# Kernel tuning notes

Measured on AMD Instinct MI355X. Metric: run time of the kernel, lower is better.

Reference implementation:

```python
import jax, jax.numpy as jnp
import numpy as np

HIDDEN = 2048
HEADS = 16
HEAD_DIM = HIDDEN // HEADS  # 128
ROPE_BASE = 10000.0
RMS_EPS = 1e-6
MINUS_INF = -10000.0


def rms_norm(x, w):
    xf = x.astype(jnp.float32)
    var = jnp.mean(xf * xf, axis=-1, keepdims=True)
    return w * (x * jax.lax.rsqrt(var + RMS_EPS))


def rotate_half(x):
    x1, x2 = jnp.split(x, 2, axis=-1)
    return jnp.concatenate((-x2, x1), axis=-1)


def rope_tables(seq_len, dtype):
    inv_freq = 1.0 / (ROPE_BASE ** (jnp.arange(0, HEAD_DIM, 2, dtype=jnp.float32) / HEAD_DIM))
    t = jnp.arange(seq_len, dtype=jnp.float32)
    freqs = jnp.einsum('i,j->ij', t, inv_freq)           # [S, D/2]
    emb = jnp.concatenate((freqs, freqs), axis=-1)       # [S, D]
    return jnp.cos(emb).astype(dtype), jnp.sin(emb).astype(dtype)


def setup_inputs() -> dict:
    key = jax.random.key(0)
    ks = jax.random.split(key, 6)
    B, S, H = 2, 2048, HIDDEN
    x = jax.random.normal(ks[0], (B, S, H), dtype=jnp.float32) * 0.5
    norm_w = jnp.ones((H,), dtype=jnp.float32)
    scale = 0.02
    wq = jax.random.normal(ks[1], (H, H), dtype=jnp.float32) * scale
    wk = jax.random.normal(ks[2], (H, H), dtype=jnp.float32) * scale
    wv = jax.random.normal(ks[3], (H, H), dtype=jnp.float32) * scale
    wo = jax.random.normal(ks[4], (H, H), dtype=jnp.float32) * scale
    position_ids = jnp.broadcast_to(jnp.arange(S, dtype=jnp.int32), (B, S))
    return {"x": x, "norm_w": norm_w, "wq": wq, "wk": wk, "wv": wv,
            "wo": wo, "position_ids": position_ids}


def reference(x, norm_w, wq, wk, wv, wo, position_ids):
    B, S, H = x.shape
    h = rms_norm(x, norm_w)
    # torch Linear: y = h @ W.T, weight is [out, in]
    def proj(w):
        return jnp.einsum('bsd,od->bso', h, w).reshape(B, S, HEADS, HEAD_DIM).transpose(0, 2, 1, 3)
    q, k, v = proj(wq), proj(wk), proj(wv)  # [B, Hh, S, D]
    cos, sin = rope_tables(S, x.dtype)
    cos = cos[position_ids][:, None]  # [B, 1, S, D]
    sin = sin[position_ids][:, None]
    q = q * cos + rotate_half(q) * sin
    k = k * cos + rotate_half(k) * sin
    scores = jnp.einsum('bhqd,bhkd->bhqk', q, k) / jnp.sqrt(jnp.float32(HEAD_DIM))
    causal = jnp.tril(jnp.ones((S, S), dtype=bool))
    scores = scores + jnp.where(causal, 0.0, MINUS_INF).astype(scores.dtype)
    probs = jax.nn.softmax(scores, axis=-1)
    ctx = jnp.einsum('bhqk,bhkd->bhqd', probs, v)          # [B, Hh, S, D]
    ctx = ctx.transpose(0, 2, 1, 3).reshape(B, S, H)
    out = jnp.einsum('bsd,od->bso', ctx, wo)
    return out
```

## Files before the change

kernel.cpp:

```cpp
#include <hip/hip_runtime.h>
#include <hip/hip_bf16.h>
#include <stdint.h>

#define S_LEN   2048
#define BATCH   2
#define HID     2048
#define NHEADS  16
#define HDIM    128
#define ROWS    (BATCH * S_LEN)
#define QKS     4096
#define ATT_SCALE 0.08838834764831843f
#define LOG2E     1.4426950408889634f

typedef __attribute__((ext_vector_type(8))) short s16x8;
typedef __attribute__((ext_vector_type(4))) float f32x4;

#define GLL16(gp, lp)                                                          \
  __builtin_amdgcn_global_load_lds(                                            \
      (__attribute__((address_space(1))) void*)(gp),                           \
      (__attribute__((address_space(3))) void*)(lp), 16, 0, 0)

__device__ __forceinline__ float bf2f(unsigned short u) {
  union { unsigned int i; float f; } v; v.i = ((unsigned int)u) << 16; return v.f;
}
__device__ __forceinline__ unsigned short f2bf(float f) {
  union { float f; unsigned int i; } v; v.f = f;
  unsigned int i = v.i;
  return (unsigned short)((i + 0x7FFFu + ((i >> 16) & 1u)) >> 16);
}
__device__ __forceinline__ void store_out(unsigned short* p, float v) { *p = f2bf(v); }
__device__ __forceinline__ void store_out(float* p, float v) { *p = v; }

__global__ __launch_bounds__(256) void cast4_kernel(const float* __restrict__ w0,
                                                    const float* __restrict__ w1,
                                                    const float* __restrict__ w2,
                                                    const float* __restrict__ w3,
                                                    unsigned short* __restrict__ dqkv,
                                                    unsigned short* __restrict__ dwo) {
  const int which = blockIdx.y;
  const float* src = (which == 0) ? w0 : (which == 1) ? w1 : (which == 2) ? w2 : w3;
  unsigned short* dst = (which < 3) ? dqkv + (size_t)which * HID * HID : dwo;
  int i = blockIdx.x * 256 + threadIdx.x;
  float4 v = ((const float4*)src)[i];
  ushort4 o;
  o.x = f2bf(v.x); o.y = f2bf(v.y); o.z = f2bf(v.z); o.w = f2bf(v.w);
  ((ushort4*)dst)[i] = o;
}

__global__ __launch_bounds__(256) void rmsnorm_kernel(const float* __restrict__ x,
                                                      const float* __restrict__ w,
                                                      unsigned short* __restrict__ h) {
  int row = blockIdx.x;
  int t = threadIdx.x;
  const float4* xr4 = (const float4*)(x + (size_t)row * HID);
  float4 a = xr4[t], b = xr4[t + 256];
  float ss = a.x*a.x + a.y*a.y + a.z*a.z + a.w*a.w
           + b.x*b.x + b.y*b.y + b.z*b.z + b.w*b.w;
#pragma unroll
  for (int off = 32; off >= 1; off >>= 1) ss += __shfl_xor(ss, off, 64);
  __shared__ float red[4];
  if ((t & 63) == 0) red[t >> 6] = ss;
  __syncthreads();
  float tot = red[0] + red[1] + red[2] + red[3];
  float rs = rsqrtf(tot * (1.0f / (float)HID) + 1e-6f);
  const float4* w4 = (const float4*)w;
  float4 wa = w4[t], wb = w4[t + 256];
  ushort4 oa, ob;
  oa.x = f2bf(a.x * wa.x * rs); oa.y = f2bf(a.y * wa.y * rs);
  oa.z = f2bf(a.z * wa.z * rs); oa.w = f2bf(a.w * wa.w * rs);
  ob.x = f2bf(b.x * wb.x * rs); ob.y = f2bf(b.y * wb.y * rs);
  ob.z = f2bf(b.z * wb.z * rs); ob.w = f2bf(b.w * wb.w * rs);
  ushort4* hr = (ushort4*)(h + (size_t)row * HID);
  hr[t] = oa; hr[t + 256] = ob;
}

__global__ void rope_tab_kernel(float* __restrict__ cost, float* __restrict__ sint) {
  int s = blockIdx.x, j = threadIdx.x;
  float inv = powf(10000.0f, -((float)j) / 64.0f);
  float ang = (float)s * inv;
  cost[s * 64 + j] = cosf(ang);
  sint[s * 64 + j] = sinf(ang);
}

__global__ __launch_bounds__(256) void rope_kernel(const int* __restrict__ pos_ids,
                                                   const float* __restrict__ cost,
                                                   const float* __restrict__ sint,
                                                   unsigned short* __restrict__ qk) {
  int row = blockIdx.x;
  int p = pos_ids[row];
  int t = threadIdx.x;
  int head = t >> 4;
  int j0 = (t & 15) * 4;
  size_t base = (size_t)row * QKS + head * HDIM;
  float4 c = *(const float4*)(cost + p * 64 + j0);
  float4 s = *(const float4*)(sint + p * 64 + j0);
#pragma unroll
  for (int which = 0; which < 2; which++) {
    unsigned short* ptr = qk + base + which * HID;
    float sc = which ? 1.0f : (ATT_SCALE * LOG2E);
    ushort4 v1 = *(ushort4*)(ptr + j0);
    ushort4 v2 = *(ushort4*)(ptr + 64 + j0);
    ushort4 o1, o2;
    o1.x = f2bf((bf2f(v1.x) * c.x - bf2f(v2.x) * s.x) * sc);
    o1.y = f2bf((bf2f(v1.y) * c.y - bf2f(v2.y) * s.y) * sc);
    o1.z = f2bf((bf2f(v1.z) * c.z - bf2f(v2.z) * s.z) * sc);
    o1.w = f2bf((bf2f(v1.w) * c.w - bf2f(v2.w) * s.w) * sc);
    o2.x = f2bf((bf2f(v2.x) * c.x + bf2f(v1.x) * s.x) * sc);
    o2.y = f2bf((bf2f(v2.y) * c.y + bf2f(v1.y) * s.y) * sc);
    o2.z = f2bf((bf2f(v2.z) * c.z + bf2f(v1.z) * s.z) * sc);
    o2.w = f2bf((bf2f(v2.w) * c.w + bf2f(v1.w) * s.w) * sc);
    *(ushort4*)(ptr + j0) = o1;
    *(ushort4*)(ptr + 64 + j0) = o2;
  }
}

#define SH(kt, bi, kk2) {                                                      \
    const unsigned short* sa_ = aQ + (size_t)(kt) * 64 + (kk2) * 32;           \
    const unsigned short* sb_ = bQ + (size_t)(kt) * 64 + (kk2) * 32;           \
    char* da_ = qsm + ((bi) * 2 + (kk2)) * 32768 + tid * 16;                   \
    GLL16(sa_, da_);                                                           \
    GLL16(sa_ + (size_t)128 * K, da_ + 8192);                                  \
    GLL16(sb_, da_ + 16384);                                                   \
    GLL16(sb_ + (size_t)128 * K, da_ + 16384 + 8192);                          \
  }

__global__ __launch_bounds__(512, 2) void gemm_qk_kernel(const unsigned short* __restrict__ A,
                                                         const unsigned short* __restrict__ B,
                                                         unsigned short* __restrict__ C,
                                                         int K, int N) {
  __shared__ __align__(16) unsigned short Qsm[2][2][2][256 * 32];
  const int bm = blockIdx.y, bn = blockIdx.x;
  const int tid = threadIdx.x;
  const int w = tid >> 6, wr = w >> 2, wc = w & 3;
  const int l = tid & 63, g = l >> 4, r = l & 15;
  const int KT = K >> 6;

  const int srow = tid >> 2;
  const int sg = (tid & 3) ^ ((tid >> 2) & 3) ^ ((tid >> 4) & 3);
  const unsigned short* aQ = A + (size_t)(bm * 256 + srow) * K + sg * 8;
  const unsigned short* bQ = B + (size_t)(bn * 256 + srow) * K + sg * 8;
  char* const qsm = (char*)Qsm;

  f32x4 zero = {0.f, 0.f, 0.f, 0.f};
  f32x4 acc[8][4];
#pragma unroll
  for (int mi = 0; mi < 8; mi++)
#pragma unroll
    for (int ni = 0; ni < 4; ni++) acc[mi][ni] = zero;

  const int ro = ((g ^ (r & 3) ^ ((r >> 2) & 3)) << 4);
  const int aOff = (wr * 128 + r) * 64 + ro;
  const int bOff = 16384 + (wc * 64 + r) * 64 + ro;

  SH(0, 0, 0); SH(0, 0, 1);

  for (int kt = 0; kt < KT; ++kt) {
    const int buf = kt & 1;
    const bool more = (kt + 1 < KT);
    const char* l0 = qsm + (buf * 2 + 0) * 32768;
    const char* l1 = qsm + (buf * 2 + 1) * 32768;

    asm volatile("s_waitcnt vmcnt(4)" ::: "memory");
    __builtin_amdgcn_s_barrier();
    __builtin_amdgcn_sched_barrier(0);
    s16x8 a[4], b[4];
#pragma unroll
    for (int ni = 0; ni < 4; ni++) b[ni] = *(const s16x8*)(l0 + bOff + ni * 1024);
#pragma unroll
    for (int i = 0; i < 4; i++) a[i] = *(const s16x8*)(l0 + aOff + i * 1024);
    if (more) SH(kt + 1, buf ^ 1, 0);
    __builtin_amdgcn_s_setprio(1);
#pragma unroll
    for (int ni = 0; ni < 4; ni++)
#pragma unroll
      for (int i = 0; i < 4; i++)
        acc[i][ni] = __builtin_amdgcn_mfma_f32_16x16x32_bf16(a[i], b[ni], acc[i][ni], 0, 0, 0);
    __builtin_amdgcn_s_setprio(0);

    s16x8 a2[4];
#pragma unroll
    for (int i = 0; i < 4; i++) a2[i] = *(const s16x8*)(l0 + aOff + (4 + i) * 1024);
    __builtin_amdgcn_s_setprio(1);
#pragma unroll
    for (int ni = 0; ni < 4; ni++)
#pragma unroll
      for (int i = 0; i < 4; i++)
        acc[4 + i][ni] = __builtin_amdgcn_mfma_f32_16x16x32_bf16(a2[i], b[ni], acc[4 + i][ni], 0, 0, 0);
    __builtin_amdgcn_s_setprio(0);

    if (more) { asm volatile("s_waitcnt vmcnt(4)" ::: "memory"); }
    else      { asm volatile("s_waitcnt vmcnt(0)" ::: "memory"); }
    __builtin_amdgcn_s_barrier();
    __builtin_amdgcn_sched_barrier(0);
#pragma unroll
    for (int ni = 0; ni < 4; ni++) b[ni] = *(const s16x8*)(l1 + bOff + ni * 1024);
#pragma unroll
    for (int i = 0; i < 4; i++) a[i] = *(const s16x8*)(l1 + aOff + i * 1024);
    if (more) SH(kt + 1, buf ^ 1, 1);
    __builtin_amdgcn_s_setprio(1);
#pragma unroll
    for (int ni = 0; ni < 4; ni++)
#pragma unroll
      for (int i = 0; i < 4; i++)
        acc[i][ni] = __builtin_amdgcn_mfma_f32_16x16x32_bf16(a[i], b[ni], acc[i][ni], 0, 0, 0);
    __builtin_amdgcn_s_setprio(0);

#pragma unroll
    for (int i = 0; i < 4; i++) a2[i] = *(const s16x8*)(l1 + aOff + (4 + i) * 1024);
    __builtin_amdgcn_s_setprio(1);
#pragma unroll
    for (int ni = 0; ni < 4; ni++)
#pragma unroll
      for (int i = 0; i < 4; i++)
        acc[4 + i][ni] = __builtin_amdgcn_mfma_f32_16x16x32_bf16(a2[i], b[ni], acc[4 + i][ni], 0, 0, 0);
    __builtin_amdgcn_s_setprio(0);
  }

#pragma unroll
  for (int mi = 0; mi < 8; mi++)
#pragma unroll
    for (int ni = 0; ni < 4; ni++) {
      const int crow = bm * 256 + wr * 128 + mi * 16 + g * 4;
      const int ccol = bn * 256 + wc * 64 + ni * 16 + r;
#pragma unroll
      for (int j = 0; j < 4; j++)
        store_out(&C[(size_t)(crow + j) * N + ccol], acc[mi][ni][j]);
    }
}
#undef SH

#define SA(kt, bi) {                                                           \
    const unsigned short* s_ = aS + (size_t)(kt) * 64;                         \
    char* d_ = (char*)Ab[bi] + tid * 16;                                       \
    GLL16(s_, d_);                                                             \
    GLL16(s_ + (size_t)64 * K, d_ + 8192);                                     \
  }
#define SB(kt, bi, hf) {                                                       \
    const unsigned short* s_ = bS + (size_t)(hf) * 128 * K + (size_t)(kt) * 64;\
    char* d_ = (char*)Bb[bi] + (hf) * 16384 + tid * 16;                        \
    GLL16(s_, d_);                                                             \
    GLL16(s_ + (size_t)64 * K, d_ + 8192);                                     \
  }

template <typename OutT, int NI, bool VT_OUT>
__global__ __launch_bounds__(512, 1) void gemm8_kernel(const unsigned short* __restrict__ A,
                                                       const unsigned short* __restrict__ B,
                                                       OutT* __restrict__ C, int K, int N) {
  __shared__ __align__(16) unsigned short Ab[3][128 * 64];
  __shared__ __align__(16) unsigned short Bb[3][NI * 64 * 64];
  const int bm = blockIdx.y, bn = blockIdx.x;
  const int tid = threadIdx.x;
  const int w = tid >> 6, wr = w >> 2, wc = w & 3;
  const int l = tid & 63, g = l >> 4, r = l & 15;
  const int KT = K >> 6;

  const int srow = tid >> 3;
  const int sgr = (tid & 7) ^ (srow & 7);
  const unsigned short* aS = A + (size_t)(bm * 128 + srow) * K + sgr * 8;
  const unsigned short* bS = B + (size_t)(bn * (NI * 64) + srow) * K + sgr * 8;

  f32x4 zero = {0.f, 0.f, 0.f, 0.f};
  f32x4 acc[4][NI];
#pragma unroll
  for (int mi = 0; mi < 4; mi++)
#pragma unroll
    for (int ni = 0; ni < NI; ni++) acc[mi][ni] = zero;

  const int swx = (r & 7) << 4;
  const int ks0 = (g << 4) ^ swx;
  const int ks1 = ((4 | g) << 4) ^ swx;
  const int aOff = (wr * 64 + r) * 128;
  const int bOff = (wc * (NI * 16) + r) * 128;

  SA(0, 0); SB(0, 0, 0); if (NI == 4) SB(0, 0, 1);
  SA(1, 1); SB(1, 1, 0); if (NI == 4) SB(1, 1, 1);

  int cur = 0;
  for (int kt = 0; kt < KT; ++kt) {
    const int b2 = (cur >= 1) ? cur - 1 : cur + 2;
    if (kt == KT - 1)      { asm volatile("s_waitcnt vmcnt(0)" ::: "memory"); }
    else if (NI == 4)      { asm volatile("s_waitcnt vmcnt(6)" ::: "memory"); }
    else                   { asm volatile("s_waitcnt vmcnt(4)" ::: "memory"); }
    __builtin_amdgcn_s_barrier();
    __builtin_amdgcn_sched_barrier(0);
    const char* lA = (const char*)Ab[cur];
    const char* lB = (const char*)Bb[cur];
    const bool more = (kt + 2 < KT);

    s16x8 a[4][2], b[NI][2];
#pragma unroll
    for (int mi = 0; mi < 4; mi++) {
      a[mi][0] = *(const s16x8*)(lA + aOff + mi * 2048 + ks0);
      a[mi][1] = *(const s16x8*)(lA + aOff + mi * 2048 + ks1);
    }
#pragma unroll
    for (int ni = 0; ni < NI / 2; ni++) {
      b[ni][0] = *(const s16x8*)(lB + bOff + ni * 2048 + ks0);
      b[ni][1] = *(const s16x8*)(lB + bOff + ni * 2048 + ks1);
    }
    if (more) { SA(kt + 2, b2); if (NI == 4) SB(kt + 2, b2, 0); }
    __builtin_amdgcn_s_setprio(1);
#pragma unroll
    for (int kk = 0; kk < 2; kk++)
#pragma unroll
      for (int ni = 0; ni < NI / 2; ni++)
#pragma unroll
        for (int mi = 0; mi < 4; mi++)
          acc[mi][ni] = __builtin_amdgcn_mfma_f32_16x16x32_bf16(a[mi][kk], b[ni][kk], acc[mi][ni], 0, 0, 0);
    __builtin_amdgcn_s_setprio(0);
    __builtin_amdgcn_sched_barrier(0);

#pragma unroll
    for (int ni = NI / 2; ni < NI; ni++) {
      b[ni][0] = *(const s16x8*)(lB + bOff + ni * 2048 + ks0);
      b[ni][1] = *(const s16x8*)(lB + bOff + ni * 2048 + ks1);
    }
    if (more) { if (NI == 4) { SB(kt + 2, b2, 1); } else { SB(kt + 2, b2, 0); } }
    __builtin_amdgcn_s_setprio(1);
#pragma unroll
    for (int kk = 0; kk < 2; kk++)
#pragma unroll
      for (int ni = NI / 2; ni < NI; ni++)
#pragma unroll
        for (int mi = 0; mi < 4; mi++)
          acc[mi][ni] = __builtin_amdgcn_mfma_f32_16x16x32_bf16(a[mi][kk], b[ni][kk], acc[mi][ni], 0, 0, 0);
    __builtin_amdgcn_s_setprio(0);
    cur = (cur == 2) ? 0 : cur + 1;
  }

#pragma unroll
  for (int mi = 0; mi < 4; mi++)
#pragma unroll
    for (int ni = 0; ni < NI; ni++) {
      const int crow = bm * 128 + wr * 64 + mi * 16 + g * 4;
      const int ccol = bn * (NI * 64) + wc * (NI * 16) + ni * 16 + r;
      if constexpr (VT_OUT) {
        const int bidx = crow >> 11;
        const int s0 = crow & (S_LEN - 1);
        const int vrow = (bidx * 16 + (ccol >> 7)) * 128 + (ccol & 127);
        ushort4 o;
        o.x = f2bf(acc[mi][ni][0]); o.y = f2bf(acc[mi][ni][1]);
        o.z = f2bf(acc[mi][ni][2]); o.w = f2bf(acc[mi][ni][3]);
        *(ushort4*)((unsigned short*)C + (size_t)vrow * S_LEN + s0) = o;
      } else {
#pragma unroll
        for (int j = 0; j < 4; j++)
          store_out(&C[(size_t)(crow + j) * N + ccol], acc[mi][ni][j]);
      }
    }
}

__global__ __launch_bounds__(256, 2) void attn_kernel(const unsigned short* __restrict__ QK,
                                                      const unsigned short* __restrict__ VT,
                                                      unsigned short* __restrict__ O) {
  __shared__ __align__(16) unsigned short Ksm[2][64 * 128];
  __shared__ __align__(16) unsigned short VTsm[2][128 * 64];
  __shared__ __align__(16) unsigned short Psm[4 * 16 * 64];
  const int bid = blockIdx.x;
  const int grp = bid & 7, idx = bid >> 3;
  const int m = idx >> 2;
  const int qt = (m < 8) ? 15 - m : m - 8;
  const int bh = (grp << 2) | (idx & 3);
  const int b = bh >> 4, hd = bh & 15;
  const int tid = threadIdx.x, w = tid >> 6, l = tid & 63, g = l >> 4, r = l & 15;
  const int qbs = qt * 128 + w * 32;

  s16x8 qf[2][4];
#pragma unroll
  for (int s = 0; s < 2; s++) {
    const unsigned short* qp = QK + (size_t)(b * S_LEN + qbs + s * 16 + r) * QKS + hd * HDIM;
#pragma unroll
    for (int ks = 0; ks < 4; ks++) qf[s][ks] = *(const s16x8*)(qp + ks * 32 + g * 8);
  }

  float mreg[2] = {-1e30f, -1e30f};
  float lregp[2] = {0.f, 0.f};
  f32x4 zero = {0.f, 0.f, 0.f, 0.f};
  f32x4 oacc[2][8];
#pragma unroll
  for (int s = 0; s < 2; s++)
#pragma unroll
    for (int di = 0; di < 8; di++) oacc[s][di] = zero;

  const int cK = tid & 15, rowK = tid >> 4;
  const unsigned short* kp_base = QK + (size_t)(b * S_LEN + rowK) * QKS + HID + hd * HDIM
                                  + ((cK ^ (rowK & 7)) << 3);
  const int cV = tid & 7, dV = tid >> 3;
  const unsigned short* vp_base = VT + (size_t)(bh * 128 + dV) * S_LEN + ((cV ^ (dV & 7)) << 3);
  char* const ksm0 = (char*)Ksm;
  char* const vtsm0 = (char*)VTsm;
  char* const psm_w = (char*)Psm + w * 2048;
  const int pswz = (r & 7) << 4;

#define STAGE(kt, bufi)                                                        \
  {                                                                            \
    const unsigned short* kp_ = kp_base + (size_t)((kt) * 64) * QKS;           \
    const unsigned short* vp_ = vp_base + (kt) * 64;                           \
    char* kd_ = ksm0 + (bufi) * 16384;                                         \
    char* vd_ = vtsm0 + (bufi) * 16384;                                        \
    GLL16(kp_,                      kd_ + tid * 16);                           \
    GLL16(kp_ + (size_t)16 * QKS,   kd_ + (tid + 256) * 16);                   \
    GLL16(kp_ + (size_t)32 * QKS,   kd_ + (tid + 512) * 16);                   \
    GLL16(kp_ + (size_t)48 * QKS,   kd_ + (tid + 768) * 16);                   \
    GLL16(vp_,                      vd_ + tid * 16);                           \
    GLL16(vp_ + (size_t)32 * S_LEN, vd_ + (tid + 256) * 16);                   \
    GLL16(vp_ + (size_t)64 * S_LEN, vd_ + (tid + 512) * 16);                   \
    GLL16(vp_ + (size_t)96 * S_LEN, vd_ + (tid + 768) * 16);                   \
  }

  const int nt = 2 * qt + 2;
  STAGE(0, 0);

  for (int kt2 = 0; kt2 < nt; kt2++) {
    const int buf = kt2 & 1;
    asm volatile("s_waitcnt vmcnt(0)" ::: "memory");
    __builtin_amdgcn_s_barrier();
    __builtin_amdgcn_sched_barrier(0);
    if (kt2 + 1 < nt) STAGE(kt2 + 1, buf ^ 1);

    const bool active = (kt2 * 64) <= (qbs + 31);
    if (active) {
      const char* ksm_c = ksm0 + buf * 16384;
      const char* vtsm_c = vtsm0 + buf * 16384;

      f32x4 sacc[2][4];
#pragma unroll
      for (int s = 0; s < 2; s++)
#pragma unroll
        for (int ni = 0; ni < 4; ni++) sacc[s][ni] = zero;
#pragma unroll
      for (int ni = 0; ni < 4; ni++) {
        const int krow = ni * 16 + r;
        const int swz = (krow & 7) << 4;
        const char* kb2 = ksm_c + krow * 256;
#pragma unroll
        for (int ks = 0; ks < 4; ks++) {
          s16x8 kf = *(const s16x8*)(kb2 + ((ks * 64 + g * 16) ^ swz));
#pragma unroll
          for (int s = 0; s < 2; s++)
            sacc[s][ni] = __builtin_amdgcn_mfma_f32_16x16x32_bf16(kf, qf[s][ks], sacc[s][ni], 0, 0, 0);
        }
      }

#pragma unroll
      for (int s = 0; s < 2; s++) {
        if ((kt2 * 64 + 63) > (qbs + s * 16)) {
#pragma unroll
          for (int ni = 0; ni < 4; ni++)
#pragma unroll
            for (int jj = 0; jj < 4; jj++)
              if ((kt2 * 64 + ni * 16 + g * 4 + jj) > (qbs + s * 16 + r)) sacc[s][ni][jj] = -1e30f;
        }
      }

      float mx[2];
#pragma unroll
      for (int s = 0; s < 2; s++) {
        float m0 = fmaxf(fmaxf(sacc[s][0][0], sacc[s][0][1]), fmaxf(sacc[s][0][2], sacc[s][0][3]));
        float m1 = fmaxf(fmaxf(sacc[s][1][0], sacc[s][1][1]), fmaxf(sacc[s][1][2], sacc[s][1][3]));
        float m2 = fmaxf(fmaxf(sacc[s][2][0], sacc[s][2][1]), fmaxf(sacc[s][2][2], sacc[s][2][3]));
        float m3 = fmaxf(fmaxf(sacc[s][3][0], sacc[s][3][1]), fmaxf(sacc[s][3][2], sacc[s][3][3]));
        float v = fmaxf(fmaxf(m0, m1), fmaxf(m2, m3));
        v = fmaxf(v, __shfl_xor(v, 16, 64));
        v = fmaxf(v, __shfl_xor(v, 32, 64));
        mx[s] = v;
      }

      bool grow = (mx[0] > mreg[0] + 8.0f) || (mx[1] > mreg[1] + 8.0f);
      if (__any(grow)) {
#pragma unroll
        for (int s = 0; s < 2; s++) {
          float mn = fmaxf(mreg[s], mx[s]);
          float corr = exp2f(mreg[s] - mn);
          mreg[s] = mn;
          lregp[s] *= corr;
#pragma unroll
          for (int di = 0; di < 8; di++) oacc[s][di] = oacc[s][di] * corr;
        }
      }

#pragma unroll
      for (int s = 0; s < 2; s++) {
#pragma unroll
        for (int ni = 0; ni < 4; ni++)
#pragma unroll
          for (int jj = 0; jj < 4; jj++) sacc[s][ni][jj] = exp2f(sacc[s][ni][jj] - mreg[s]);
        float s0 = (sacc[s][0][0] + sacc[s][0][1]) + (sacc[s][0][2] + sacc[s][0][3]);
        float s1 = (sacc[s][1][0] + sacc[s][1][1]) + (sacc[s][1][2] + sacc[s][1][3]);
        float s2 = (sacc[s][2][0] + sacc[s][2][1]) + (sacc[s][2][2] + sacc[s][2][3]);
        float s3 = (sacc[s][3][0] + sacc[s][3][1]) + (sacc[s][3][2] + sacc[s][3][3]);
        lregp[s] += (s0 + s1) + (s2 + s3);
      }

#pragma unroll
      for (int s = 0; s < 2; s++) {
#pragma unroll
        for (int ni = 0; ni < 4; ni++) {
          unsigned int pk01, pk23;
          asm("v_cvt_pk_bf16_f32 %0, %1, %2" : "=v"(pk01) : "v"(sacc[s][ni][0]), "v"(sacc[s][ni][1]));
          asm("v_cvt_pk_bf16_f32 %0, %1, %2" : "=v"(pk23) : "v"(sacc[s][ni][2]), "v"(sacc[s][ni][3]));
          uint2 pk; pk.x = pk01; pk.y = pk23;
          *(uint2*)(psm_w + ((r * 128 + ni * 32 + g * 8) ^ pswz)) = pk;
        }
#pragma unroll
        for (int ksl = 0; ksl < 2; ksl++) {
          s16x8 pb = *(const s16x8*)(psm_w + ((r * 128 + ksl * 64 + g * 16) ^ pswz));
          const int kgran = ksl * 4 + g;
#pragma unroll
          for (int di = 0; di < 8; di++) {
            const int d = di * 16 + r;
            s16x8 vf = *(const s16x8*)(vtsm_c + d * 128 + ((kgran ^ (d & 7)) << 4));
            oacc[s][di] = __builtin_amdgcn_mfma_f32_16x16x32_bf16(vf, pb, oacc[s][di], 0, 0, 0);
          }
        }
      }
    }
  }
#undef STAGE

#pragma unroll
  for (int s = 0; s < 2; s++) {
    float lsum = lregp[s];
    lsum += __shfl_xor(lsum, 16, 64);
    lsum += __shfl_xor(lsum, 32, 64);
    const float inv = 1.0f / lsum;
    unsigned short* orow = O + (size_t)(b * S_LEN + qbs + s * 16 + r) * HID + hd * HDIM;
#pragma unroll
    for (int di = 0; di < 8; di++) {
      ushort4 o;
      o.x = f2bf(oacc[s][di][0] * inv); o.y = f2bf(oacc[s][di][1] * inv);
      o.z = f2bf(oacc[s][di][2] * inv); o.w = f2bf(oacc[s][di][3] * inv);
      *(ushort4*)(orow + di * 16 + g * 4) = o;
    }
  }
}

extern "C" void kernel_launch(void* const* d_in, const int* in_sizes, int n_in,
                              void* d_out, int out_size, void* d_ws, size_t ws_size,
                              hipStream_t stream) {
  const float* x      = (const float*)d_in[0];
  const float* norm_w = (const float*)d_in[1];
  const float* wq     = (const float*)d_in[2];
  const float* wk     = (const float*)d_in[3];
  const float* wv     = (const float*)d_in[4];
  const float* wo     = (const float*)d_in[5];
  const int*   pos    = (const int*)d_in[6];
  float* out = (float*)d_out;

  char* ws = (char*)d_ws;
  const size_t WQKV_B = (size_t)3 * HID * HID * 2;
  const size_t WO_B   = (size_t)HID * HID * 2;
  const size_t H_B    = (size_t)ROWS * HID * 2;
  const size_t QK_B   = (size_t)ROWS * QKS * 2;

  unsigned short* wqkvb = (unsigned short*)(ws);
  unsigned short* vt    = (unsigned short*)(ws);
  unsigned short* wob   = (unsigned short*)(ws + WQKV_B);
  unsigned short* h     = (unsigned short*)(ws + WQKV_B + WO_B);
  unsigned short* qk    = (unsigned short*)(ws + WQKV_B + WO_B + H_B);
  float* cost = (float*)(ws + WQKV_B + WO_B + H_B + QK_B);
  float* sint = cost + (size_t)S_LEN * 64;

  dim3 cgrid(HID * HID / 4 / 256, 4);
  cast4_kernel<<<cgrid, 256, 0, stream>>>(wq, wk, wv, wo, wqkvb, wob);
  rope_tab_kernel<<<S_LEN, 64, 0, stream>>>(cost, sint);
  rmsnorm_kernel<<<ROWS, 256, 0, stream>>>(x, norm_w, h);

  dim3 qkgrid(2 * HID / 256, ROWS / 256);
  gemm_qk_kernel<<<qkgrid, 512, 0, stream>>>(h, wqkvb, qk, HID, QKS);

  dim3 vgrid(HID / 256, ROWS / 128);
  gemm8_kernel<unsigned short, 4, true><<<vgrid, 512, 0, stream>>>(
      h, wqkvb + (size_t)2 * HID * HID, vt, HID, S_LEN);

  rope_kernel<<<ROWS, 256, 0, stream>>>(pos, cost, sint, qk);

  attn_kernel<<<512, 256, 0, stream>>>(qk, vt, h );

  dim3 ogrid(HID / 256, ROWS / 128);
  gemm8_kernel<float, 4, false><<<ogrid, 512, 0, stream>>>(h, wob, out, HID, HID);
}
```

Baseline: 263.3 us.

## Fuse rope table into cast kernel, precompute attention LDS offsets, simplify scheduling

```diff
diff --git a/kernel.cpp b/kernel.cpp
--- a/kernel.cpp
+++ b/kernel.cpp
@@ -11,6 +11,7 @@
 #define QKS     4096
 #define ATT_SCALE 0.08838834764831843f
 #define LOG2E     1.4426950408889634f
+#define LOG2_10000 13.287712379549449f
 
 typedef __attribute__((ext_vector_type(8))) short s16x8;
 typedef __attribute__((ext_vector_type(4))) float f32x4;
@@ -30,14 +31,29 @@
 }
 __device__ __forceinline__ void store_out(unsigned short* p, float v) { *p = f2bf(v); }
 __device__ __forceinline__ void store_out(float* p, float v) { *p = v; }
-
-__global__ __launch_bounds__(256) void cast4_kernel(const float* __restrict__ w0,
+__device__ __forceinline__ float fmax3(float a, float b, float c) {
+  return fmaxf(fmaxf(a, b), c);
+}
+
+__global__ __launch_bounds__(256) void cast5_kernel(const float* __restrict__ w0,
                                                     const float* __restrict__ w1,
                                                     const float* __restrict__ w2,
                                                     const float* __restrict__ w3,
                                                     unsigned short* __restrict__ dqkv,
-                                                    unsigned short* __restrict__ dwo) {
+                                                    unsigned short* __restrict__ dwo,
+                                                    float* __restrict__ ropetab) {
   const int which = blockIdx.y;
+  if (which == 4) {
+    int s = blockIdx.x, j = threadIdx.x;
+    if (s < S_LEN && j < 64) {
+      float inv = exp2f(-((float)j) * (LOG2_10000 / 64.0f));
+      float ang = (float)s * inv;
+      float2 cs;
+      __sincosf(ang, &cs.y, &cs.x);
+      *(float2*)(ropetab + (s * 64 + j) * 2) = cs;
+    }
+    return;
+  }
   const float* src = (which == 0) ? w0 : (which == 1) ? w1 : (which == 2) ? w2 : w3;
   unsigned short* dst = (which < 3) ? dqkv + (size_t)which * HID * HID : dwo;
   int i = blockIdx.x * 256 + threadIdx.x;
@@ -74,17 +90,8 @@
   hr[t] = oa; hr[t + 256] = ob;
 }
 
-__global__ void rope_tab_kernel(float* __restrict__ cost, float* __restrict__ sint) {
-  int s = blockIdx.x, j = threadIdx.x;
-  float inv = powf(10000.0f, -((float)j) / 64.0f);
-  float ang = (float)s * inv;
-  cost[s * 64 + j] = cosf(ang);
-  sint[s * 64 + j] = sinf(ang);
-}
-
 __global__ __launch_bounds__(256) void rope_kernel(const int* __restrict__ pos_ids,
-                                                   const float* __restrict__ cost,
-                                                   const float* __restrict__ sint,
+                                                   const float* __restrict__ tab,
                                                    unsigned short* __restrict__ qk) {
   int row = blockIdx.x;
   int p = pos_ids[row];
@@ -92,8 +99,10 @@
   int head = t >> 4;
   int j0 = (t & 15) * 4;
   size_t base = (size_t)row * QKS + head * HDIM;
-  float4 c = *(const float4*)(cost + p * 64 + j0);
-  float4 s = *(const float4*)(sint + p * 64 + j0);
+  float4 cs01 = *(const float4*)(tab + (p * 64 + j0) * 2);
+  float4 cs23 = *(const float4*)(tab + (p * 64 + j0 + 2) * 2);
+  float4 c = {cs01.x, cs01.z, cs23.x, cs23.z};
+  float4 s = {cs01.y, cs01.w, cs23.y, cs23.w};
 #pragma unroll
   for (int which = 0; which < 2; which++) {
     unsigned short* ptr = qk + base + which * HID;
@@ -359,7 +368,7 @@
   const int bid = blockIdx.x;
   const int grp = bid & 7, idx = bid >> 3;
   const int m = idx >> 2;
-  const int qt = (m < 8) ? 15 - m : m - 8;
+  const int qt = 15 - m;
   const int bh = (grp << 2) | (idx & 3);
   const int b = bh >> 4, hd = bh & 15;
   const int tid = threadIdx.x, w = tid >> 6, l = tid & 63, g = l >> 4, r = l & 15;
@@ -389,8 +398,18 @@
   const unsigned short* vp_base = VT + (size_t)(bh * 128 + dV) * S_LEN + ((cV ^ (dV & 7)) << 3);
   char* const ksm0 = (char*)Ksm;
   char* const vtsm0 = (char*)VTsm;
-  char* const psm_w = (char*)Psm + w * 2048;
-  const int pswz = (r & 7) << 4;
+  const int sw8 = (r & 7) << 4;
+  int kc[4], pcw[4], pcr[2], vc[2];
+#pragma unroll
+  for (int ks = 0; ks < 4; ks++) kc[ks] = (ks * 64 + g * 16) ^ sw8;
+#pragma unroll
+  for (int ni = 0; ni < 4; ni++) pcw[ni] = (ni * 32 + g * 8) ^ sw8;
+#pragma unroll
+  for (int ksl = 0; ksl < 2; ksl++) {
+    pcr[ksl] = (ksl * 64 + g * 16) ^ sw8;
+    vc[ksl] = ((ksl * 4 + g) ^ (r & 7)) << 4;
+  }
+  char* const pT = (char*)Psm + w * 2048 + r * 128;
 
 #define STAGE(kt, bufi)                                                        \
   {                                                                            \
@@ -420,8 +439,8 @@
 
     const bool active = (kt2 * 64) <= (qbs + 31);
     if (active) {
-      const char* ksm_c = ksm0 + buf * 16384;
-      const char* vtsm_c = vtsm0 + buf * 16384;
+      const char* kT = ksm0 + buf * 16384 + r * 256;
+      const char* vT = vtsm0 + buf * 16384 + r * 128;
 
       f32x4 sacc[2][4];
 #pragma unroll
@@ -429,13 +448,11 @@
 #pragma unroll
         for (int ni = 0; ni < 4; ni++) sacc[s][ni] = zero;
 #pragma unroll
-      for (int ni = 0; ni < 4; ni++) {
-        const int krow = ni * 16 + r;
-        const int swz = (krow & 7) << 4;
-        const char* kb2 = ksm_c + krow * 256;
-#pragma unroll
-        for (int ks = 0; ks < 4; ks++) {
-          s16x8 kf = *(const s16x8*)(kb2 + ((ks * 64 + g * 16) ^ swz));
+      for (int ks = 0; ks < 4; ks++) {
+        const char* kp2 = kT + kc[ks];
+#pragma unroll
+        for (int ni = 0; ni < 4; ni++) {
+          s16x8 kf = *(const s16x8*)(kp2 + ni * 4096);
 #pragma unroll
           for (int s = 0; s < 2; s++)
             sacc[s][ni] = __builtin_amdgcn_mfma_f32_16x16x32_bf16(kf, qf[s][ks], sacc[s][ni], 0, 0, 0);
@@ -445,22 +462,25 @@
 #pragma unroll
       for (int s = 0; s < 2; s++) {
         if ((kt2 * 64 + 63) > (qbs + s * 16)) {
+          const int qg = qbs + s * 16 + r - kt2 * 64 - g * 4;
 #pragma unroll
           for (int ni = 0; ni < 4; ni++)
 #pragma unroll
             for (int jj = 0; jj < 4; jj++)
-              if ((kt2 * 64 + ni * 16 + g * 4 + jj) > (qbs + s * 16 + r)) sacc[s][ni][jj] = -1e30f;
+              if ((ni * 16 + jj) > qg) sacc[s][ni][jj] = -1e30f;
         }
       }
 
       float mx[2];
 #pragma unroll
       for (int s = 0; s < 2; s++) {
-        float m0 = fmaxf(fmaxf(sacc[s][0][0], sacc[s][0][1]), fmaxf(sacc[s][0][2], sacc[s][0][3]));
-        float m1 = fmaxf(fmaxf(sacc[s][1][0], sacc[s][1][1]), fmaxf(sacc[s][1][2], sacc[s][1][3]));
-        float m2 = fmaxf(fmaxf(sacc[s][2][0], sacc[s][2][1]), fmaxf(sacc[s][2][2], sacc[s][2][3]));
-        float m3 = fmaxf(fmaxf(sacc[s][3][0], sacc[s][3][1]), fmaxf(sacc[s][3][2], sacc[s][3][3]));
-        float v = fmaxf(fmaxf(m0, m1), fmaxf(m2, m3));
+        float ma = fmax3(fmax3(sacc[s][0][0], sacc[s][0][1], sacc[s][0][2]),
+                         fmax3(sacc[s][0][3], sacc[s][1][0], sacc[s][1][1]),
+                         fmax3(sacc[s][1][2], sacc[s][1][3], sacc[s][2][0]));
+        float mb = fmax3(fmax3(sacc[s][2][1], sacc[s][2][2], sacc[s][2][3]),
+                         fmax3(sacc[s][3][0], sacc[s][3][1], sacc[s][3][2]),
+                         sacc[s][3][3]);
+        float v = fmaxf(ma, mb);
         v = fmaxf(v, __shfl_xor(v, 16, 64));
         v = fmaxf(v, __shfl_xor(v, 32, 64));
         mx[s] = v;
@@ -500,16 +520,15 @@
           asm("v_cvt_pk_bf16_f32 %0, %1, %2" : "=v"(pk01) : "v"(sacc[s][ni][0]), "v"(sacc[s][ni][1]));
           asm("v_cvt_pk_bf16_f32 %0, %1, %2" : "=v"(pk23) : "v"(sacc[s][ni][2]), "v"(sacc[s][ni][3]));
           uint2 pk; pk.x = pk01; pk.y = pk23;
-          *(uint2*)(psm_w + ((r * 128 + ni * 32 + g * 8) ^ pswz)) = pk;
+          *(uint2*)(pT + pcw[ni]) = pk;
         }
 #pragma unroll
         for (int ksl = 0; ksl < 2; ksl++) {
-          s16x8 pb = *(const s16x8*)(psm_w + ((r * 128 + ksl * 64 + g * 16) ^ pswz));
-          const int kgran = ksl * 4 + g;
+          s16x8 pb = *(const s16x8*)(pT + pcr[ksl]);
+          const char* vp2 = vT + vc[ksl];
 #pragma unroll
           for (int di = 0; di < 8; di++) {
-            const int d = di * 16 + r;
-            s16x8 vf = *(const s16x8*)(vtsm_c + d * 128 + ((kgran ^ (d & 7)) << 4));
+            s16x8 vf = *(const s16x8*)(vp2 + di * 2048);
             oacc[s][di] = __builtin_amdgcn_mfma_f32_16x16x32_bf16(vf, pb, oacc[s][di], 0, 0, 0);
           }
         }
@@ -558,12 +577,10 @@
   unsigned short* wob   = (unsigned short*)(ws + WQKV_B);
   unsigned short* h     = (unsigned short*)(ws + WQKV_B + WO_B);
   unsigned short* qk    = (unsigned short*)(ws + WQKV_B + WO_B + H_B);
-  float* cost = (float*)(ws + WQKV_B + WO_B + H_B + QK_B);
-  float* sint = cost + (size_t)S_LEN * 64;
-
-  dim3 cgrid(HID * HID / 4 / 256, 4);
-  cast4_kernel<<<cgrid, 256, 0, stream>>>(wq, wk, wv, wo, wqkvb, wob);
-  rope_tab_kernel<<<S_LEN, 64, 0, stream>>>(cost, sint);
+  float* ropetab = (float*)(ws + WQKV_B + WO_B + H_B + QK_B);
+
+  dim3 cgrid(HID * HID / 4 / 256, 5);
+  cast5_kernel<<<cgrid, 256, 0, stream>>>(wq, wk, wv, wo, wqkvb, wob, ropetab);
   rmsnorm_kernel<<<ROWS, 256, 0, stream>>>(x, norm_w, h);
 
   dim3 qkgrid(2 * HID / 256, ROWS / 256);
@@ -573,7 +590,7 @@
   gemm8_kernel<unsigned short, 4, true><<<vgrid, 512, 0, stream>>>(
       h, wqkvb + (size_t)2 * HID * HID, vt, HID, S_LEN);
 
-  rope_kernel<<<ROWS, 256, 0, stream>>>(pos, cost, sint, qk);
+  rope_kernel<<<ROWS, 256, 0, stream>>>(pos, ropetab, qk);
 
   attn_kernel<<<512, 256, 0, stream>>>(qk, vt, h );
 
```

Result: no change. 259.9 us (-1.3%).
